# Optimization experiments

Measured on AMD Instinct MI355X. Metric: run time of the kernel, lower is better.

Reference implementation:

```python
import jax, jax.numpy as jnp
import numpy as np

D_MODEL = 2048
N_HEADS = 16
KV_HEADS = 4
HEAD_DIM = D_MODEL // N_HEADS            # 128
GROUP = N_HEADS // KV_HEADS              # 4
KV_WIDTH = KV_HEADS * HEAD_DIM           # 512
B, T = 2, 2048


def setup_inputs() -> dict:
    key = jax.random.key(0)
    ks = jax.random.split(key, 5)
    s = 0.02
    x = jax.random.normal(ks[0], (B, T, D_MODEL), dtype=jnp.float32)
    attn_mask = jnp.tril(jnp.ones((T, T), dtype=bool))  # causal
    qkv_w = jax.random.normal(ks[1], (D_MODEL, D_MODEL + 2 * KV_WIDTH), dtype=jnp.float32) * s
    qkv_b = jax.random.normal(ks[2], (D_MODEL + 2 * KV_WIDTH,), dtype=jnp.float32) * s
    proj_w = jax.random.normal(ks[3], (D_MODEL, D_MODEL), dtype=jnp.float32) * s
    proj_b = jax.random.normal(ks[4], (D_MODEL,), dtype=jnp.float32) * s
    return {"x": x, "attn_mask": attn_mask, "qkv_w": qkv_w, "qkv_b": qkv_b,
            "proj_w": proj_w, "proj_b": proj_b}


def reference(x, attn_mask, qkv_w, qkv_b, proj_w, proj_b):
    b, t, c = x.shape
    qkv = x @ qkv_w + qkv_b                               # [b,t,3072]
    q = qkv[..., :D_MODEL]
    k = qkv[..., D_MODEL:D_MODEL + KV_WIDTH]
    v = qkv[..., D_MODEL + KV_WIDTH:]
    # q: [b, kv_heads, group, t, d]; k,v: [b, kv_heads, t, d]
    q = q.reshape(b, t, KV_HEADS, GROUP, HEAD_DIM).transpose(0, 2, 3, 1, 4)
    k = k.reshape(b, t, KV_HEADS, HEAD_DIM).transpose(0, 2, 1, 3)
    v = v.reshape(b, t, KV_HEADS, HEAD_DIM).transpose(0, 2, 1, 3)
    scale = 1.0 / jnp.sqrt(jnp.asarray(HEAD_DIM, dtype=x.dtype))
    att = jnp.einsum('bkgtd,bksd->bkgts', q, k) * scale   # [b,kv,g,t,t]
    att = jnp.where(attn_mask, att, jnp.asarray(-jnp.inf, dtype=att.dtype))
    att = jax.nn.softmax(att, axis=-1)
    out = jnp.einsum('bkgts,bksd->bkgtd', att, v)         # [b,kv,g,t,d]
    out = out.transpose(0, 3, 1, 2, 4).reshape(b, t, c)
    return out @ proj_w + proj_b
```

## Files before the change

kernel.cpp:

```cpp
#include <hip/hip_runtime.h>
#include <cstdint>
#include <cstddef>

#define D_MODEL 2048
#define T_SEQ   2048
#define BATCH   2
#define N_HEADS 16
#define KV_HEADS 4
#define HEAD_DIM 128
#define QKV_N   3072
#define ROWS    (BATCH * T_SEQ)

typedef float  floatx4 __attribute__((ext_vector_type(4)));
typedef short  shortx8 __attribute__((ext_vector_type(8)));
typedef __bf16 bf16x8  __attribute__((ext_vector_type(8)));

typedef const void __attribute__((address_space(1))) gvoid_t;
typedef void __attribute__((address_space(3)))       svoid_t;

__device__ __forceinline__ floatx4 mfma16(shortx8 a, shortx8 b, floatx4 c) {
  return __builtin_amdgcn_mfma_f32_16x16x32_bf16(
      __builtin_bit_cast(bf16x8, a), __builtin_bit_cast(bf16x8, b), c, 0, 0, 0);
}

__device__ __forceinline__ unsigned short f2bf(float f) {
  union { float f; unsigned int u; } v; v.f = f;
  unsigned int u = v.u;
  u += 0x7fffu + ((u >> 16) & 1u);
  return (unsigned short)(u >> 16);
}

__global__ void cvt_x(const float* __restrict__ in, unsigned short* __restrict__ out, int n4) {
  int i = blockIdx.x * blockDim.x + threadIdx.x;
  if (i >= n4) return;
  float4 v = ((const float4*)in)[i];
  ushort4 o;
  o.x = f2bf(v.x); o.y = f2bf(v.y); o.z = f2bf(v.z); o.w = f2bf(v.w);
  ((ushort4*)out)[i] = o;
}

__global__ void transpose_cvt(const float* __restrict__ W, unsigned short* __restrict__ Wt,
                              int K, int N) {
  __shared__ float tile[32][33];
  int n0 = blockIdx.x * 32, k0 = blockIdx.y * 32;
  int tx = threadIdx.x, ty = threadIdx.y;
  #pragma unroll
  for (int i = 0; i < 32; i += 8)
    tile[ty + i][tx] = W[(size_t)(k0 + ty + i) * N + n0 + tx];
  __syncthreads();
  #pragma unroll
  for (int i = 0; i < 32; i += 8)
    Wt[(size_t)(n0 + ty + i) * K + k0 + tx] = f2bf(tile[tx][ty + i]);
}

__global__ void build_kt(const unsigned short* __restrict__ qkv, unsigned short* __restrict__ kst) {
  int o = blockIdx.x * blockDim.x + threadIdx.x;
  int t   = o & 2047;
  int d8  = (o >> 11) & 15;
  int kvh = (o >> 15) & 3;
  int b   = o >> 17;
  uint4 v = *(const uint4*)(qkv + (size_t)(b * T_SEQ + t) * QKV_N
                            + D_MODEL + kvh * HEAD_DIM + d8 * 8);
  *(uint4*)(kst + (size_t)o * 8) = v;
}

__global__ void build_vt(const unsigned short* __restrict__ qkv, unsigned short* __restrict__ vst) {
  int o = blockIdx.x * blockDim.x + threadIdx.x;
  int d   = o & 127;
  int t8  = (o >> 7) & 255;
  int kvh = (o >> 15) & 3;
  int b   = o >> 17;
  const unsigned short* src = qkv + (size_t)(b * T_SEQ + t8 * 8) * QKV_N
                              + D_MODEL + 512 + kvh * HEAD_DIM + d;
  union { unsigned short s[8]; uint4 v; } tmp;
  #pragma unroll
  for (int j = 0; j < 8; ++j) tmp.s[j] = src[(size_t)j * QKV_N];
  *(uint4*)(vst + (size_t)o * 8) = tmp.v;
}

__global__ __launch_bounds__(512, 2) void gemm256(
    const unsigned short* __restrict__ A,
    const unsigned short* __restrict__ Bt,
    const float* __restrict__ bias,
    void* __restrict__ Cout,
    int M, int N, int K, int c_bf16)
{
  __shared__ __align__(16) unsigned short lds[65536];
  const int tid  = threadIdx.x;
  const int wave = tid >> 6, lane = tid & 63;
  const int quad = lane >> 4, l16 = lane & 15;
  const int wr = wave >> 2, wc = wave & 3;
  const int bm = blockIdx.y * 256, bn = blockIdx.x * 256;
  const int NT = K >> 6;

  const int r0 = tid >> 3;
  const int cx = (tid & 7) ^ (r0 & 7);
  const size_t K64 = (size_t)64 * K;
  const unsigned short* a_src = A  + (size_t)(bm + r0) * K + cx * 8;
  const unsigned short* b_src = Bt + (size_t)(bn + r0) * K + cx * 8;
  const int wOff = wave * 512;

  #define LDSA_(buf, half) (lds + (((buf) << 1) + (half)) * 8192)
  #define LDSB_(buf, half) (lds + 32768 + (((buf) << 1) + (half)) * 8192)
  #define KOFF(h, t) ((size_t)(h) * 128 * K + (size_t)(t) * 64)
  #define STAGE(srcbase, ldshalf, koff) do {                                          \
    __builtin_amdgcn_global_load_lds((gvoid_t*)((srcbase) + (koff)),                  \
        (svoid_t*)((ldshalf) + wOff), 16, 0, 0);                                      \
    __builtin_amdgcn_global_load_lds((gvoid_t*)((srcbase) + (koff) + K64),            \
        (svoid_t*)((ldshalf) + wOff + 4096), 16, 0, 0);                               \
  } while (0)

  const int rowA = (wr * 64 + l16) * 64;
  const int rowB = (wc * 32 + l16) * 64;
  const int xo0 = ((quad)     ^ (l16 & 7)) * 8;
  const int xo1 = ((4 + quad) ^ (l16 & 7)) * 8;

  floatx4 acc[8][4] = {};
  shortx8 Afr[4][2];
  shortx8 Bfr[4][2];

  STAGE(a_src, LDSA_(0, 0), KOFF(0, 0));
  STAGE(b_src, LDSB_(0, 0), KOFF(0, 0));
  STAGE(b_src, LDSB_(0, 1), KOFF(1, 0));
  STAGE(a_src, LDSA_(0, 1), KOFF(1, 0));
  if (NT > 1) {
    STAGE(a_src, LDSA_(1, 0), KOFF(0, 1));
    STAGE(b_src, LDSB_(1, 0), KOFF(0, 1));
    STAGE(b_src, LDSB_(1, 1), KOFF(1, 1));
  }

  for (int t = 0; t < NT; ++t) {
    const int buf = t & 1;
    unsigned short* sA0 = LDSA_(buf, 0);
    unsigned short* sA1 = LDSA_(buf, 1);
    unsigned short* sB0 = LDSB_(buf, 0);
    unsigned short* sB1 = LDSB_(buf, 1);

    if (t == NT - 1) asm volatile("s_waitcnt vmcnt(0)" ::: "memory");
    else             asm volatile("s_waitcnt vmcnt(6)" ::: "memory");
    __builtin_amdgcn_s_barrier();
    #pragma unroll
    for (int mi = 0; mi < 4; ++mi) {
      Afr[mi][0] = *(const shortx8*)(sA0 + rowA + mi * 1024 + xo0);
      Afr[mi][1] = *(const shortx8*)(sA0 + rowA + mi * 1024 + xo1);
    }
    #pragma unroll
    for (int ni = 0; ni < 2; ++ni) {
      Bfr[ni][0] = *(const shortx8*)(sB0 + rowB + ni * 1024 + xo0);
      Bfr[ni][1] = *(const shortx8*)(sB0 + rowB + ni * 1024 + xo1);
    }
    if (t + 1 < NT) STAGE(a_src, LDSA_(buf ^ 1, 1), KOFF(1, t + 1));
    asm volatile("s_waitcnt lgkmcnt(0)" ::: "memory");
    __builtin_amdgcn_s_setprio(1);
    #pragma unroll
    for (int ks = 0; ks < 2; ++ks)
      #pragma unroll
      for (int mi = 0; mi < 4; ++mi)
        #pragma unroll
        for (int ni = 0; ni < 2; ++ni)
          acc[mi][ni] = mfma16(Afr[mi][ks], Bfr[ni][ks], acc[mi][ni]);
    __builtin_amdgcn_s_setprio(0);
    __builtin_amdgcn_s_barrier();

    #pragma unroll
    for (int ni = 0; ni < 2; ++ni) {
      Bfr[2 + ni][0] = *(const shortx8*)(sB1 + rowB + ni * 1024 + xo0);
      Bfr[2 + ni][1] = *(const shortx8*)(sB1 + rowB + ni * 1024 + xo1);
    }
    if (t + 2 < NT) STAGE(a_src, LDSA_(buf, 0), KOFF(0, t + 2));
    __builtin_amdgcn_s_barrier();
    asm volatile("s_waitcnt lgkmcnt(0)" ::: "memory");
    __builtin_amdgcn_s_setprio(1);
    #pragma unroll
    for (int ks = 0; ks < 2; ++ks)
      #pragma unroll
      for (int mi = 0; mi < 4; ++mi)
        #pragma unroll
        for (int ni = 0; ni < 2; ++ni)
          acc[mi][2 + ni] = mfma16(Afr[mi][ks], Bfr[2 + ni][ks], acc[mi][2 + ni]);
    __builtin_amdgcn_s_setprio(0);
    __builtin_amdgcn_s_barrier();

    #pragma unroll
    for (int mi = 0; mi < 4; ++mi) {
      Afr[mi][0] = *(const shortx8*)(sA1 + rowA + mi * 1024 + xo0);
      Afr[mi][1] = *(const shortx8*)(sA1 + rowA + mi * 1024 + xo1);
    }
    if (t + 2 < NT) STAGE(b_src, LDSB_(buf, 0), KOFF(0, t + 2));
    __builtin_amdgcn_s_barrier();
    asm volatile("s_waitcnt lgkmcnt(0)" ::: "memory");
    __builtin_amdgcn_s_setprio(1);
    #pragma unroll
    for (int ks = 0; ks < 2; ++ks)
      #pragma unroll
      for (int mi = 0; mi < 4; ++mi)
        #pragma unroll
        for (int ni = 0; ni < 2; ++ni)
          acc[4 + mi][2 + ni] = mfma16(Afr[mi][ks], Bfr[2 + ni][ks], acc[4 + mi][2 + ni]);
    __builtin_amdgcn_s_setprio(0);
    __builtin_amdgcn_s_barrier();

    if (t + 2 < NT) STAGE(b_src, LDSB_(buf, 1), KOFF(1, t + 2));
    __builtin_amdgcn_s_barrier();
    __builtin_amdgcn_s_setprio(1);
    #pragma unroll
    for (int ks = 0; ks < 2; ++ks)
      #pragma unroll
      for (int mi = 0; mi < 4; ++mi)
        #pragma unroll
        for (int ni = 0; ni < 2; ++ni)
          acc[4 + mi][ni] = mfma16(Afr[mi][ks], Bfr[ni][ks], acc[4 + mi][ni]);
    __builtin_amdgcn_s_setprio(0);
    __builtin_amdgcn_s_barrier();
  }

  #pragma unroll
  for (int mi = 0; mi < 8; ++mi) {
    const int row = bm + (mi >> 2) * 128 + wr * 64 + (mi & 3) * 16 + quad * 4;
    #pragma unroll
    for (int ni = 0; ni < 4; ++ni) {
      const int col = bn + (ni >> 1) * 128 + wc * 32 + (ni & 1) * 16 + l16;
      const float bv = bias[col];
      #pragma unroll
      for (int r = 0; r < 4; ++r) {
        float v = acc[mi][ni][r] + bv;
        if (c_bf16)
          ((unsigned short*)Cout)[(size_t)(row + r) * N + col] = f2bf(v);
        else
          ((float*)Cout)[(size_t)(row + r) * N + col] = v;
      }
    }
  }
  #undef LDSA_
  #undef LDSB_
  #undef KOFF
  #undef STAGE
}

__global__ __launch_bounds__(256) void attn_kernel(
    const unsigned short* __restrict__ qkv,
    const unsigned short* __restrict__ kst,
    const unsigned short* __restrict__ vst,
    unsigned short* __restrict__ aout)
{
  __shared__ __align__(16) unsigned short sK[16 * 64 * 8];
  __shared__ __align__(16) unsigned short sV[8 * 128 * 8];
  __shared__ __align__(16) unsigned short sP[4][8 * 16 * 8];

  const int tid  = threadIdx.x;
  const int wave = tid >> 6, lane = tid & 63;
  const int quad = lane >> 4, l16 = lane & 15;
  const int head = blockIdx.y, b = blockIdx.z;
  const int kvh = head >> 2;
  const float cf = 0.08838834764831845f * 1.4426950408889634f;

  const unsigned short* kbase = kst + (size_t)((b * KV_HEADS + kvh) * 16) * 2048 * 8;
  const unsigned short* vbase = vst + (size_t)((b * KV_HEADS + kvh) * 256) * 128 * 8;
  unsigned short* sPw = sP[wave];

  #pragma unroll 1
  for (int half = 0; half < 2; ++half) {
    const int qt = half ? blockIdx.x : (31 - blockIdx.x);
    const int q0 = qt * 64;

    shortx8 qf[4];
    {
      const unsigned short* qp = qkv + (size_t)(b * T_SEQ + q0 + wave * 16 + l16) * QKV_N
                                 + head * HEAD_DIM + quad * 8;
      #pragma unroll
      for (int ks = 0; ks < 4; ++ks)
        qf[ks] = *(const shortx8*)(qp + ks * 32);
    }

    float m_i[4], l_i[4];
    #pragma unroll
    for (int r = 0; r < 4; ++r) { m_i[r] = -__builtin_inff(); l_i[r] = 0.f; }
    floatx4 o_acc[8] = {};

    for (int kt = 0; kt <= qt; ++kt) {
      const int kb = kt * 64;

      __syncthreads();
      #pragma unroll
      for (int it = 0; it < 4; ++it) {
        const int c = it * 4 + wave;
        __builtin_amdgcn_global_load_lds(
            (gvoid_t*)(kbase + ((size_t)c * 2048 + kb) * 8 + lane * 8),
            (svoid_t*)(sK + c * 512), 16, 0, 0);
      }
      const unsigned short* vtile = vbase + (size_t)(kb >> 3) * 128 * 8;
      #pragma unroll
      for (int it = 0; it < 4; ++it) {
        const int c = it * 4 + wave;
        __builtin_amdgcn_global_load_lds(
            (gvoid_t*)(vtile + c * 512 + lane * 8),
            (svoid_t*)(sV + c * 512), 16, 0, 0);
      }
      __syncthreads();

      floatx4 s[4] = {};
      #pragma unroll
      for (int ks = 0; ks < 4; ++ks) {
        #pragma unroll
        for (int ct = 0; ct < 4; ++ct) {
          shortx8 kf = *(const shortx8*)&sK[((ks * 4 + quad) * 64 + ct * 16 + l16) * 8];
          s[ct] = mfma16(qf[ks], kf, s[ct]);
        }
      }

      if (kt == qt) {
        const int qrow = q0 + wave * 16 + quad * 4;
        #pragma unroll
        for (int ct = 0; ct < 4; ++ct) {
          const int kcol = kb + ct * 16 + l16;
          #pragma unroll
          for (int r = 0; r < 4; ++r)
            if (kcol > qrow + r) s[ct][r] = -__builtin_inff();
        }
      }

      float alpha_r[4];
      #pragma unroll
      for (int r = 0; r < 4; ++r) {
        float mx = fmaxf(fmaxf(s[0][r], s[1][r]), fmaxf(s[2][r], s[3][r]));
        mx = fmaxf(mx, __shfl_xor(mx, 1));
        mx = fmaxf(mx, __shfl_xor(mx, 2));
        mx = fmaxf(mx, __shfl_xor(mx, 4));
        mx = fmaxf(mx, __shfl_xor(mx, 8));
        const float newm = fmaxf(m_i[r], mx);
        const float nmc = newm * cf;
        float p0 = exp2f(fmaf(s[0][r], cf, -nmc));
        float p1 = exp2f(fmaf(s[1][r], cf, -nmc));
        float p2 = exp2f(fmaf(s[2][r], cf, -nmc));
        float p3 = exp2f(fmaf(s[3][r], cf, -nmc));
        s[0][r] = p0; s[1][r] = p1; s[2][r] = p2; s[3][r] = p3;
        const float alpha = exp2f(fmaf(m_i[r], cf, -nmc));
        alpha_r[r] = alpha;
        l_i[r] = l_i[r] * alpha + ((p0 + p1) + (p2 + p3));
        m_i[r] = newm;
      }
      if (__ballot(alpha_r[0] < 1.f || alpha_r[1] < 1.f ||
                   alpha_r[2] < 1.f || alpha_r[3] < 1.f)) {
        #pragma unroll
        for (int nt = 0; nt < 8; ++nt)
          #pragma unroll
          for (int r = 0; r < 4; ++r) o_acc[nt][r] *= alpha_r[r];
      }

      #pragma unroll
      for (int ct = 0; ct < 4; ++ct)
        #pragma unroll
        for (int r = 0; r < 4; ++r)
          sPw[((ct * 2 + (l16 >> 3)) * 16 + quad * 4 + r) * 8 + (l16 & 7)] = f2bf(s[ct][r]);
      __asm__ __volatile__("s_waitcnt lgkmcnt(0)" ::: "memory");

      #pragma unroll
      for (int ks = 0; ks < 2; ++ks) {
        shortx8 pf = *(const shortx8*)&sPw[((ks * 4 + quad) * 16 + l16) * 8];
        #pragma unroll
        for (int nt = 0; nt < 8; ++nt) {
          shortx8 vf = *(const shortx8*)&sV[((ks * 4 + quad) * 128 + nt * 16 + l16) * 8];
          o_acc[nt] = mfma16(pf, vf, o_acc[nt]);
        }
      }
    }

    const int trow = q0 + wave * 16 + quad * 4;
    #pragma unroll
    for (int r = 0; r < 4; ++r) {
      float l = l_i[r];
      l += __shfl_xor(l, 1);
      l += __shfl_xor(l, 2);
      l += __shfl_xor(l, 4);
      l += __shfl_xor(l, 8);
      const float inv = 1.f / l;
      #pragma unroll
      for (int nt = 0; nt < 8; ++nt) {
        aout[(size_t)(b * T_SEQ + trow + r) * D_MODEL + head * HEAD_DIM + nt * 16 + l16] =
            f2bf(o_acc[nt][r] * inv);
      }
    }
  }
}

extern "C" void kernel_launch(void* const* d_in, const int* in_sizes, int n_in,
                              void* d_out, int out_size, void* d_ws, size_t ws_size,
                              hipStream_t stream) {
  const float* x      = (const float*)d_in[0];
  const float* qkv_w  = (const float*)d_in[2];
  const float* qkv_b  = (const float*)d_in[3];
  const float* proj_w = (const float*)d_in[4];
  const float* proj_b = (const float*)d_in[5];
  float* out = (float*)d_out;

  char* ws = (char*)d_ws;
  unsigned short* x_bf    = (unsigned short*)(ws);
  unsigned short* qkvw_t  = (unsigned short*)(ws + (size_t)16777216);
  unsigned short* projw_t = (unsigned short*)(ws + (size_t)29360128);
  unsigned short* qkvbuf  = (unsigned short*)(ws + (size_t)37748736);
  unsigned short* vstaged = (unsigned short*)(ws + (size_t)62914560);
  unsigned short* kstaged = qkvw_t;
  unsigned short* attn_out = x_bf;

  cvt_x<<<(ROWS * D_MODEL / 4 + 255) / 256, 256, 0, stream>>>(x, x_bf, ROWS * D_MODEL / 4);
  transpose_cvt<<<dim3(QKV_N / 32, D_MODEL / 32), dim3(32, 8), 0, stream>>>(qkv_w, qkvw_t, D_MODEL, QKV_N);
  transpose_cvt<<<dim3(D_MODEL / 32, D_MODEL / 32), dim3(32, 8), 0, stream>>>(proj_w, projw_t, D_MODEL, D_MODEL);
  gemm256<<<dim3(QKV_N / 256, ROWS / 256), 512, 0, stream>>>(
      x_bf, qkvw_t, qkv_b, (void*)qkvbuf, ROWS, QKV_N, D_MODEL, 1);
  build_kt<<<1024, 256, 0, stream>>>(qkvbuf, kstaged);
  build_vt<<<1024, 256, 0, stream>>>(qkvbuf, vstaged);
  attn_kernel<<<dim3(16, N_HEADS, BATCH), 256, 0, stream>>>(qkvbuf, kstaged, vstaged, attn_out);
  gemm256<<<dim3(D_MODEL / 256, ROWS / 256), 512, 0, stream>>>(
      attn_out, projw_t, proj_b, (void*)out, ROWS, D_MODEL, D_MODEL, 0);
}
```

Before: 350.5 us.

## Split attention into one q-tile per block, lazy rescale, hardware bf16 convert

The attention grid doubles to 32 blocks per head, each handling one query tile instead of a paired long/short tile. This gives 1024 blocks for better occupancy, but work per block becomes unbalanced, so scheduling order now matters. Online-softmax rescaling is deferred until the running max grows by more than a threshold (the FA4-style lazy rescale), which skips most alpha multiplies on the output accumulator. Software bf16 rounding is replaced with the hardware conversion in the GEMM epilogue, the P store and the output.

```diff
diff --git a/kernel.cpp b/kernel.cpp
--- a/kernel.cpp
+++ b/kernel.cpp
@@ -28,6 +28,10 @@
   unsigned int u = v.u;
   u += 0x7fffu + ((u >> 16) & 1u);
   return (unsigned short)(u >> 16);
+}
+
+__device__ __forceinline__ unsigned short f2bf_hw(float f) {
+  return __builtin_bit_cast(unsigned short, (__bf16)f);
 }
 
 __global__ void cvt_x(const float* __restrict__ in, unsigned short* __restrict__ out, int n4) {
@@ -225,7 +229,7 @@
       for (int r = 0; r < 4; ++r) {
         float v = acc[mi][ni][r] + bv;
         if (c_bf16)
-          ((unsigned short*)Cout)[(size_t)(row + r) * N + col] = f2bf(v);
+          ((unsigned short*)Cout)[(size_t)(row + r) * N + col] = f2bf_hw(v);
         else
           ((float*)Cout)[(size_t)(row + r) * N + col] = v;
       }
@@ -253,132 +257,140 @@
   const int head = blockIdx.y, b = blockIdx.z;
   const int kvh = head >> 2;
   const float cf = 0.08838834764831845f * 1.4426950408889634f;
+  const float THR = 25.0f;
 
   const unsigned short* kbase = kst + (size_t)((b * KV_HEADS + kvh) * 16) * 2048 * 8;
   const unsigned short* vbase = vst + (size_t)((b * KV_HEADS + kvh) * 256) * 128 * 8;
   unsigned short* sPw = sP[wave];
 
-  #pragma unroll 1
-  for (int half = 0; half < 2; ++half) {
-    const int qt = half ? blockIdx.x : (31 - blockIdx.x);
-    const int q0 = qt * 64;
-
-    shortx8 qf[4];
-    {
-      const unsigned short* qp = qkv + (size_t)(b * T_SEQ + q0 + wave * 16 + l16) * QKV_N
-                                 + head * HEAD_DIM + quad * 8;
-      #pragma unroll
-      for (int ks = 0; ks < 4; ++ks)
-        qf[ks] = *(const shortx8*)(qp + ks * 32);
-    }
-
-    float m_i[4], l_i[4];
-    #pragma unroll
-    for (int r = 0; r < 4; ++r) { m_i[r] = -__builtin_inff(); l_i[r] = 0.f; }
-    floatx4 o_acc[8] = {};
-
-    for (int kt = 0; kt <= qt; ++kt) {
-      const int kb = kt * 64;
-
-      __syncthreads();
-      #pragma unroll
-      for (int it = 0; it < 4; ++it) {
-        const int c = it * 4 + wave;
-        __builtin_amdgcn_global_load_lds(
-            (gvoid_t*)(kbase + ((size_t)c * 2048 + kb) * 8 + lane * 8),
-            (svoid_t*)(sK + c * 512), 16, 0, 0);
+  const int qt = 31 - blockIdx.x;
+  const int q0 = qt * 64;
+
+  shortx8 qf[4];
+  {
+    const unsigned short* qp = qkv + (size_t)(b * T_SEQ + q0 + wave * 16 + l16) * QKV_N
+                               + head * HEAD_DIM + quad * 8;
+    #pragma unroll
+    for (int ks = 0; ks < 4; ++ks)
+      qf[ks] = *(const shortx8*)(qp + ks * 32);
+  }
+
+  float m_i[4], l_i[4];
+  #pragma unroll
+  for (int r = 0; r < 4; ++r) { m_i[r] = -__builtin_inff(); l_i[r] = 0.f; }
+  floatx4 o_acc[8] = {};
+
+  for (int kt = 0; kt <= qt; ++kt) {
+    const int kb = kt * 64;
+
+    __syncthreads();
+    #pragma unroll
+    for (int it = 0; it < 4; ++it) {
+      const int c = it * 4 + wave;
+      __builtin_amdgcn_global_load_lds(
+          (gvoid_t*)(kbase + ((size_t)c * 2048 + kb) * 8 + lane * 8),
+          (svoid_t*)(sK + c * 512), 16, 0, 0);
+    }
+    const unsigned short* vtile = vbase + (size_t)(kb >> 3) * 128 * 8;
+    #pragma unroll
+    for (int it = 0; it < 4; ++it) {
+      const int c = it * 4 + wave;
+      __builtin_amdgcn_global_load_lds(
+          (gvoid_t*)(vtile + c * 512 + lane * 8),
+          (svoid_t*)(sV + c * 512), 16, 0, 0);
+    }
+    __syncthreads();
+
+    floatx4 s[4] = {};
+    #pragma unroll
+    for (int ks = 0; ks < 4; ++ks) {
+      #pragma unroll
+      for (int ct = 0; ct < 4; ++ct) {
+        shortx8 kf = *(const shortx8*)&sK[((ks * 4 + quad) * 64 + ct * 16 + l16) * 8];
+        s[ct] = mfma16(qf[ks], kf, s[ct]);
       }
-      const unsigned short* vtile = vbase + (size_t)(kb >> 3) * 128 * 8;
-      #pragma unroll
-      for (int it = 0; it < 4; ++it) {
-        const int c = it * 4 + wave;
-        __builtin_amdgcn_global_load_lds(
-            (gvoid_t*)(vtile + c * 512 + lane * 8),
-            (svoid_t*)(sV + c * 512), 16, 0, 0);
+    }
+
+    if (kt == qt) {
+      const int qrow = q0 + wave * 16 + quad * 4;
+      #pragma unroll
+      for (int ct = 0; ct < 4; ++ct) {
+        const int kcol = kb + ct * 16 + l16;
+        #pragma unroll
+        for (int r = 0; r < 4; ++r)
+          if (kcol > qrow + r) s[ct][r] = -__builtin_inff();
       }
-      __syncthreads();
-
-      floatx4 s[4] = {};
-      #pragma unroll
-      for (int ks = 0; ks < 4; ++ks) {
-        #pragma unroll
-        for (int ct = 0; ct < 4; ++ct) {
-          shortx8 kf = *(const shortx8*)&sK[((ks * 4 + quad) * 64 + ct * 16 + l16) * 8];
-          s[ct] = mfma16(qf[ks], kf, s[ct]);
-        }
+    }
+
+    float mx[4];
+    #pragma unroll
+    for (int r = 0; r < 4; ++r) {
+      float m = fmaxf(fmaxf(s[0][r], s[1][r]), fmaxf(s[2][r], s[3][r]));
+      m = fmaxf(m, __shfl_xor(m, 1));
+      m = fmaxf(m, __shfl_xor(m, 2));
+      m = fmaxf(m, __shfl_xor(m, 4));
+      m = fmaxf(m, __shfl_xor(m, 8));
+      mx[r] = m;
+    }
+
+    if (__ballot((mx[0] > m_i[0] + THR) || (mx[1] > m_i[1] + THR) ||
+                 (mx[2] > m_i[2] + THR) || (mx[3] > m_i[3] + THR))) {
+      float alpha_r[4];
+      #pragma unroll
+      for (int r = 0; r < 4; ++r) {
+        const float newm = fmaxf(m_i[r], mx[r]);
+        alpha_r[r] = exp2f((m_i[r] - newm) * cf);
+        m_i[r] = newm;
+        l_i[r] *= alpha_r[r];
       }
-
-      if (kt == qt) {
-        const int qrow = q0 + wave * 16 + quad * 4;
-        #pragma unroll
-        for (int ct = 0; ct < 4; ++ct) {
-          const int kcol = kb + ct * 16 + l16;
-          #pragma unroll
-          for (int r = 0; r < 4; ++r)
-            if (kcol > qrow + r) s[ct][r] = -__builtin_inff();
-        }
+      #pragma unroll
+      for (int nt = 0; nt < 8; ++nt)
+        #pragma unroll
+        for (int r = 0; r < 4; ++r) o_acc[nt][r] *= alpha_r[r];
+    }
+
+    #pragma unroll
+    for (int r = 0; r < 4; ++r) {
+      const float nmc = m_i[r] * cf;
+      float p0 = exp2f(fmaf(s[0][r], cf, -nmc));
+      float p1 = exp2f(fmaf(s[1][r], cf, -nmc));
+      float p2 = exp2f(fmaf(s[2][r], cf, -nmc));
+      float p3 = exp2f(fmaf(s[3][r], cf, -nmc));
+      s[0][r] = p0; s[1][r] = p1; s[2][r] = p2; s[3][r] = p3;
+      l_i[r] += (p0 + p1) + (p2 + p3);
+    }
+
+    #pragma unroll
+    for (int ct = 0; ct < 4; ++ct)
+      #pragma unroll
+      for (int r = 0; r < 4; ++r)
+        sPw[((ct * 2 + (l16 >> 3)) * 16 + quad * 4 + r) * 8 + (l16 & 7)] = f2bf_hw(s[ct][r]);
+    __asm__ __volatile__("s_waitcnt lgkmcnt(0)" ::: "memory");
+
+    #pragma unroll
+    for (int ks = 0; ks < 2; ++ks) {
+      shortx8 pf = *(const shortx8*)&sPw[((ks * 4 + quad) * 16 + l16) * 8];
+      #pragma unroll
+      for (int nt = 0; nt < 8; ++nt) {
+        shortx8 vf = *(const shortx8*)&sV[((ks * 4 + quad) * 128 + nt * 16 + l16) * 8];
+        o_acc[nt] = mfma16(pf, vf, o_acc[nt]);
       }
-
-      float alpha_r[4];
-      #pragma unroll
-      for (int r = 0; r < 4; ++r) {
-        float mx = fmaxf(fmaxf(s[0][r], s[1][r]), fmaxf(s[2][r], s[3][r]));
-        mx = fmaxf(mx, __shfl_xor(mx, 1));
-        mx = fmaxf(mx, __shfl_xor(mx, 2));
-        mx = fmaxf(mx, __shfl_xor(mx, 4));
-        mx = fmaxf(mx, __shfl_xor(mx, 8));
-        const float newm = fmaxf(m_i[r], mx);
-        const float nmc = newm * cf;
-        float p0 = exp2f(fmaf(s[0][r], cf, -nmc));
-        float p1 = exp2f(fmaf(s[1][r], cf, -nmc));
-        float p2 = exp2f(fmaf(s[2][r], cf, -nmc));
-        float p3 = exp2f(fmaf(s[3][r], cf, -nmc));
-        s[0][r] = p0; s[1][r] = p1; s[2][r] = p2; s[3][r] = p3;
-        const float alpha = exp2f(fmaf(m_i[r], cf, -nmc));
-        alpha_r[r] = alpha;
-        l_i[r] = l_i[r] * alpha + ((p0 + p1) + (p2 + p3));
-        m_i[r] = newm;
-      }
-      if (__ballot(alpha_r[0] < 1.f || alpha_r[1] < 1.f ||
-                   alpha_r[2] < 1.f || alpha_r[3] < 1.f)) {
-        #pragma unroll
-        for (int nt = 0; nt < 8; ++nt)
-          #pragma unroll
-          for (int r = 0; r < 4; ++r) o_acc[nt][r] *= alpha_r[r];
-      }
-
-      #pragma unroll
-      for (int ct = 0; ct < 4; ++ct)
-        #pragma unroll
-        for (int r = 0; r < 4; ++r)
-          sPw[((ct * 2 + (l16 >> 3)) * 16 + quad * 4 + r) * 8 + (l16 & 7)] = f2bf(s[ct][r]);
-      __asm__ __volatile__("s_waitcnt lgkmcnt(0)" ::: "memory");
-
-      #pragma unroll
-      for (int ks = 0; ks < 2; ++ks) {
-        shortx8 pf = *(const shortx8*)&sPw[((ks * 4 + quad) * 16 + l16) * 8];
-        #pragma unroll
-        for (int nt = 0; nt < 8; ++nt) {
-          shortx8 vf = *(const shortx8*)&sV[((ks * 4 + quad) * 128 + nt * 16 + l16) * 8];
-          o_acc[nt] = mfma16(pf, vf, o_acc[nt]);
-        }
-      }
-    }
-
-    const int trow = q0 + wave * 16 + quad * 4;
-    #pragma unroll
-    for (int r = 0; r < 4; ++r) {
-      float l = l_i[r];
-      l += __shfl_xor(l, 1);
-      l += __shfl_xor(l, 2);
-      l += __shfl_xor(l, 4);
-      l += __shfl_xor(l, 8);
-      const float inv = 1.f / l;
-      #pragma unroll
-      for (int nt = 0; nt < 8; ++nt) {
-        aout[(size_t)(b * T_SEQ + trow + r) * D_MODEL + head * HEAD_DIM + nt * 16 + l16] =
-            f2bf(o_acc[nt][r] * inv);
-      }
+    }
+  }
+
+  const int trow = q0 + wave * 16 + quad * 4;
+  #pragma unroll
+  for (int r = 0; r < 4; ++r) {
+    float l = l_i[r];
+    l += __shfl_xor(l, 1);
+    l += __shfl_xor(l, 2);
+    l += __shfl_xor(l, 4);
+    l += __shfl_xor(l, 8);
+    const float inv = 1.f / l;
+    #pragma unroll
+    for (int nt = 0; nt < 8; ++nt) {
+      aout[(size_t)(b * T_SEQ + trow + r) * D_MODEL + head * HEAD_DIM + nt * 16 + l16] =
+          f2bf_hw(o_acc[nt][r] * inv);
     }
   }
 }
@@ -409,7 +421,7 @@
       x_bf, qkvw_t, qkv_b, (void*)qkvbuf, ROWS, QKV_N, D_MODEL, 1);
   build_kt<<<1024, 256, 0, stream>>>(qkvbuf, kstaged);
   build_vt<<<1024, 256, 0, stream>>>(qkvbuf, vstaged);
-  attn_kernel<<<dim3(16, N_HEADS, BATCH), 256, 0, stream>>>(qkvbuf, kstaged, vstaged, attn_out);
+  attn_kernel<<<dim3(32, N_HEADS, BATCH), 256, 0, stream>>>(qkvbuf, kstaged, vstaged, attn_out);
   gemm256<<<dim3(D_MODEL / 256, ROWS / 256), 512, 0, stream>>>(
       attn_out, projw_t, proj_b, (void*)out, ROWS, D_MODEL, D_MODEL, 0);
 }
```

Measured after the change: 409.1 us. 16.7% more time.
